# Optimization experiments

Hardware: AMD Instinct MI355X
Metric: run time of the kernel (lower is better)

## Reference

```python
import jax, jax.numpy as jnp
import numpy as np

H = 512; V = 100; V1 = V + 1; T = 20; L = 2; B = 1024; M = 5; K = 10; DFF = 4 * H
NEG = -1e9


def _ln(x, g, b):
    m = x.mean(-1, keepdims=True)
    v = x.var(-1, keepdims=True)
    return (x - m) / jnp.sqrt(v + 1e-5) * g + b


def _attn(q_in, kv_in, iw, ib, ow, ob, mask):
    # single-head attention, inputs [T,B,H] / [S,B,H]
    q = q_in @ iw[:H].T + ib[:H]
    k = kv_in @ iw[H:2 * H].T + ib[H:2 * H]
    v = kv_in @ iw[2 * H:].T + ib[2 * H:]
    s = jnp.einsum('qbh,kbh->bqk', q, k) / jnp.sqrt(jnp.float32(H))
    if mask is not None:
        s = s + mask
    a = jax.nn.softmax(s, axis=-1)
    o = jnp.einsum('bqk,kbh->qbh', a, v)
    return o @ ow.T + ob


def _pos_encoding(max_len, d):
    pos = jnp.arange(max_len, dtype=jnp.float32)[:, None]
    div = jnp.exp(jnp.arange(0, d, 2, dtype=jnp.float32) * (-np.log(10000.0) / d))
    pe = jnp.zeros((max_len, d), jnp.float32)
    pe = pe.at[:, 0::2].set(jnp.sin(pos * div)).at[:, 1::2].set(jnp.cos(pos * div))
    return pe[:, None, :]  # [T,1,H]


def setup_inputs() -> dict:
    key = jax.random.key(0)
    ks = jax.random.split(key, 20)
    s = 0.05
    rn = lambda k, shape: jax.random.normal(k, shape, jnp.float32) * s
    return dict(
        meanings=jax.random.randint(ks[0], (B, M), 0, K),
        emb_table=rn(ks[1], (M * K, H)),
        v2e_w=rn(ks[2], (H, V1)), v2e_b=rn(ks[3], (H,)),
        e2v_w=rn(ks[4], (V1, H)), e2v_b=rn(ks[5], (V1,)),
        sa_in_w=rn(ks[6], (L, 3 * H, H)), sa_in_b=rn(ks[7], (L, 3 * H)),
        sa_out_w=rn(ks[8], (L, H, H)), sa_out_b=rn(ks[9], (L, H)),
        ca_in_w=rn(ks[10], (L, 3 * H, H)), ca_in_b=rn(ks[11], (L, 3 * H)),
        ca_out_w=rn(ks[12], (L, H, H)), ca_out_b=rn(ks[13], (L, H)),
        ff1_w=rn(ks[14], (L, DFF, H)), ff1_b=rn(ks[15], (L, DFF)),
        ff2_w=rn(ks[16], (L, H, DFF)), ff2_b=rn(ks[17], (L, H)),
        ln_g=jnp.ones((L, 3, H), jnp.float32),
        ln_b=jnp.zeros((L, 3, H), jnp.float32),
    )


def reference(meanings, emb_table, v2e_w, v2e_b, e2v_w, e2v_b,
              sa_in_w, sa_in_b, sa_out_w, sa_out_b,
              ca_in_w, ca_in_b, ca_out_w, ca_out_b,
              ff1_w, ff1_b, ff2_w, ff2_b, ln_g, ln_b):
    bsz = meanings.shape[0]
    # meanings_offset = (cumsum(ones)-1)*K == arange(M)*K
    idx = meanings + jnp.arange(M) * K          # [B,M]
    src = emb_table[idx].sum(axis=1)[None]      # [1,B,H] memory
    pe = _pos_encoding(T, H)
    # start token one-hot probabilities
    probs = jnp.zeros((1, bsz, V1), jnp.float32).at[:, :, V].set(1.0)
    outs = []
    for i in range(T):
        x = probs @ v2e_w.T + v2e_b + pe[:i + 1]            # [i+1,B,H]
        mask = jnp.triu(jnp.full((i + 1, i + 1), NEG, jnp.float32), k=1)
        for l in range(L):
            x = _ln(x + _attn(x, x, sa_in_w[l], sa_in_b[l], sa_out_w[l], sa_out_b[l], mask),
                    ln_g[l, 0], ln_b[l, 0])
            x = _ln(x + _attn(x, src, ca_in_w[l], ca_in_b[l], ca_out_w[l], ca_out_b[l], None),
                    ln_g[l, 1], ln_b[l, 1])
            ff = jax.nn.relu(x @ ff1_w[l].T + ff1_b[l]) @ ff2_w[l].T + ff2_b[l]
            x = _ln(x + ff, ln_g[l, 2], ln_b[l, 2])
        logits = x @ e2v_w.T + e2v_b                        # [i+1,B,V1]
        last = logits[-1]                                   # [B,V1]
        outs.append(last)
        probs = jnp.concatenate([probs, jax.nn.softmax(last, axis=-1)[None]], axis=0)
    return jnp.stack(outs, axis=0)                          # [T,B,V1]
```

## Files before the change

### kernel.cpp

```cpp
#include <hip/hip_runtime.h>
#include <hip/hip_bf16.h>
#include <math.h>

#define Hdim 512
#define Vv   100
#define V1n  101
#define Tt   20
#define Ln   2
#define Bb   1024
#define Mm   5
#define Kk   10
#define DFFn 2048

typedef _Float16 f16;
typedef __attribute__((ext_vector_type(8))) _Float16 f16x8;
typedef __attribute__((ext_vector_type(16))) float f32x16;

static const size_t BH  = (size_t)Bb * Hdim;
static const size_t PSP = (size_t)Bb * 128;

__device__ __forceinline__ void split2(float v, f16* s) {
    f16 h0 = (f16)v;
    float r = v - (float)h0;
    s[0] = h0; s[1] = (f16)r;
}
__device__ __forceinline__ void xsp_write(f16* __restrict__ xsp, int row, int h, float v)
{
    f16 s[2]; split2(v, s);
    size_t o = (size_t)(h >> 3) * 8192 + (size_t)row * 8 + (h & 7);
    xsp[o] = s[0]; xsp[BH + o] = s[1];
}

template<int EPI>
__global__ __launch_bounds__(256, 2) void gemm_sp(
    const f16* __restrict__ Asp, const f16* __restrict__ Wsp,
    const float* __restrict__ bias,
    float* __restrict__ C, f16* __restrict__ Csp, size_t cplane,
    int N, int Kd, int kcount, int posn)
{
    __shared__ f16 lds[16384];
    const int tid = threadIdx.x;
    const int lane = tid & 63, w = tid >> 6;
    const int wm = w >> 1, wn = w & 1;
    const int bm = blockIdx.y * 128, bn = blockIdx.x * 128;
    const int kc0 = blockIdx.z * (kcount >> 3);
    const int nt = kcount >> 5;
    const int K8 = Kd >> 3;

    size_t gA[4], gB[4]; int lA[4], lB[4];
#pragma unroll
    for (int q = 0; q < 4; ++q) {
        int cid = q * 256 + tid, slab = cid >> 7, win = cid & 127;
        int p = slab >> 2, kcr = slab & 3;
        gA[q] = ((size_t)p * K8 + kc0 + kcr) * 8192 + (size_t)bm * 8 + win * 8;
        lA[q] = slab * 1024 + win * 8;
        gB[q] = ((size_t)p * K8 + kc0 + kcr) * ((size_t)N * 8) + (size_t)bn * 8 + win * 8;
        lB[q] = 8192 + slab * 1024 + win * 8;
    }

    f32x16 acc[2][2];
#pragma unroll
    for (int mi = 0; mi < 2; ++mi)
#pragma unroll
        for (int ni = 0; ni < 2; ++ni)
#pragma unroll
            for (int j = 0; j < 16; ++j) acc[mi][ni][j] = 0.f;

    f16x8 rA[4], rB[4];
#pragma unroll
    for (int q = 0; q < 4; ++q) {
        rA[q] = *(const f16x8*)(Asp + gA[q]);
        rB[q] = *(const f16x8*)(Wsp + gB[q]);
    }

    for (int t = 0; t < nt; ++t) {
        __syncthreads();
#pragma unroll
        for (int q = 0; q < 4; ++q) {
            *(f16x8*)&lds[lA[q]] = rA[q];
            *(f16x8*)&lds[lB[q]] = rB[q];
        }
        __syncthreads();
        if (t + 1 < nt) {
#pragma unroll
            for (int q = 0; q < 4; ++q) {
                rA[q] = *(const f16x8*)(Asp + gA[q] + (size_t)(t + 1) * 32768);
                rB[q] = *(const f16x8*)(Wsp + gB[q] + (size_t)(t + 1) * 32 * N);
            }
        }
#pragma unroll
        for (int ks = 0; ks < 2; ++ks) {
            const int kb = (2 * ks + (lane >> 5)) * 1024 + (lane & 31) * 8;
            f16x8 a[2][2], b[2][2];
#pragma unroll
            for (int mi = 0; mi < 2; ++mi)
#pragma unroll
                for (int p = 0; p < 2; ++p)
                    a[mi][p] = *(const f16x8*)&lds[p * 4096 + kb + (64 * wm + 32 * mi) * 8];
#pragma unroll
            for (int ni = 0; ni < 2; ++ni)
#pragma unroll
                for (int p = 0; p < 2; ++p)
                    b[ni][p] = *(const f16x8*)&lds[8192 + p * 4096 + kb + (64 * wn + 32 * ni) * 8];
#pragma unroll
            for (int mi = 0; mi < 2; ++mi)
#pragma unroll
                for (int ni = 0; ni < 2; ++ni) {
                    f32x16 v = acc[mi][ni];
                    v = __builtin_amdgcn_mfma_f32_32x32x16_f16(a[mi][1], b[ni][0], v, 0, 0, 0);
                    v = __builtin_amdgcn_mfma_f32_32x32x16_f16(a[mi][0], b[ni][1], v, 0, 0, 0);
                    v = __builtin_amdgcn_mfma_f32_32x32x16_f16(a[mi][0], b[ni][0], v, 0, 0, 0);
                    acc[mi][ni] = v;
                }
        }
    }

    const int er0 = bm + 64 * wm + 4 * (lane >> 5);
    const int ec0 = bn + 64 * wn + (lane & 31);
#pragma unroll
    for (int mi = 0; mi < 2; ++mi) {
#pragma unroll
        for (int ni = 0; ni < 2; ++ni) {
            int col = ec0 + 32 * ni;
#pragma unroll
            for (int r = 0; r < 16; ++r) {
                int row = er0 + 32 * mi + (r & 3) + 8 * (r >> 2);
                float v = acc[mi][ni][r];
                if (EPI == 0) {
                    C[(size_t)blockIdx.z * Bb * N + (size_t)row * N + col] = v;
                } else if (EPI == 1) {
                    v = fmaxf(v + bias[col], 0.f);
                    f16 s[2]; split2(v, s);
                    size_t o = (size_t)(col >> 3) * 8192 + (size_t)row * 8 + (col & 7);
                    Csp[o] = s[0]; Csp[cplane + o] = s[1];
                } else if (EPI == 3) {
                    v += bias[col];
                    f16 s[2]; split2(v, s);
                    size_t o = (size_t)(col >> 3) * 8192 + (size_t)row * 8 + (col & 7);
                    Csp[o] = s[0]; Csp[cplane + o] = s[1];
                } else if (EPI == 4) {
                    C[(size_t)row * N + col] = v + bias[col];
                } else if (EPI == 5) {
                    v += bias[col];
                    int j2 = col & ~1;
                    float div = expf(-(float)j2 * (logf(10000.f) / (float)Hdim));
                    float ang = (float)posn * div;
                    v += (col & 1) ? cosf(ang) : sinf(ang);
                    C[(size_t)row * Hdim + col] = v;
                    f16 s[2]; split2(v, s);
                    size_t o = (size_t)(col >> 3) * 8192 + (size_t)row * 8 + (col & 7);
                    Csp[o] = s[0]; Csp[cplane + o] = s[1];
                }
            }
        }
    }
}

__global__ void split_mat(const float* __restrict__ src, f16* __restrict__ dst,
                          int Nreal, int Npad, int Kreal, int kpl)
{
    int i = blockIdx.x * 256 + threadIdx.x;
    int Kpad = 1 << kpl;
    if (i >= (Npad << kpl)) return;
    int n = i >> kpl, k = i & (Kpad - 1);
    float v = (n < Nreal && k < Kreal) ? src[(size_t)n * Kreal + k] : 0.f;
    f16 s[2]; split2(v, s);
    size_t plane = (size_t)Npad << kpl;
    size_t o = (size_t)(k >> 3) * ((size_t)Npad * 8) + (size_t)n * 8 + (k & 7);
    dst[o] = s[0]; dst[plane + o] = s[1];
}

__global__ void src_kernel(const int* __restrict__ meanings,
                           const float* __restrict__ emb, f16* __restrict__ ssp)
{
    int idx = blockIdx.x * 256 + threadIdx.x;
    int b = idx >> 9, h = idx & 511;
    float s = 0.f;
#pragma unroll
    for (int m = 0; m < Mm; ++m) {
        int row = meanings[b * Mm + m] + m * Kk;
        s += emb[(size_t)row * Hdim + h];
    }
    xsp_write(ssp, b, h, s);
}

__global__ void init_x(const float* __restrict__ v2e_w, const float* __restrict__ v2e_b,
                       float* __restrict__ x, f16* __restrict__ xsp)
{
    int idx = blockIdx.x * 256 + threadIdx.x;
    int b = idx >> 9, h = idx & 511;
    float s = v2e_w[(size_t)h * V1n + Vv] + v2e_b[h] + ((h & 1) ? 1.f : 0.f);
    x[idx] = s;
    xsp_write(xsp, b, h, s);
}

__global__ __launch_bounds__(256) void attn_fused(
    const float* __restrict__ P, const float* __restrict__ bias3h,
    float* __restrict__ kc, float* __restrict__ vc,
    f16* __restrict__ osplit, int step)
{
    __shared__ float qs[Hdim];
    __shared__ float ssm[32];
    __shared__ float wts[32];
    int b = blockIdx.x, tid = threadIdx.x, lane = tid & 63, wv = tid >> 6;
    const size_t PS = (size_t)Bb * 1536;
    const float* pb = P + (size_t)b * 1536;
#pragma unroll
    for (int c0 = 0; c0 < 2; ++c0) {
        int c = tid + c0 * 256;
        float qv = bias3h[c]        + pb[c]        + pb[PS + c];
        float kv = bias3h[512 + c]  + pb[512 + c]  + pb[PS + 512 + c];
        float vv = bias3h[1024 + c] + pb[1024 + c] + pb[PS + 1024 + c];
        qs[c] = qv;
        kc[((size_t)step * Bb + b) * Hdim + c] = kv;
        vc[((size_t)step * Bb + b) * Hdim + c] = vv;
    }
    __syncthreads();
    const float4* q4 = (const float4*)qs;
    for (int t = wv; t <= step; t += 4) {
        const float4* k4 = (const float4*)(kc + ((size_t)t * Bb + b) * Hdim);
        float4 qa = q4[lane], ka = k4[lane];
        float4 qb = q4[lane + 64], kb = k4[lane + 64];
        float p = qa.x*ka.x + qa.y*ka.y + qa.z*ka.z + qa.w*ka.w
                + qb.x*kb.x + qb.y*kb.y + qb.z*kb.z + qb.w*kb.w;
#pragma unroll
        for (int off = 32; off; off >>= 1) p += __shfl_down(p, off);
        if (!lane) ssm[t] = p * 0.044194173824159216f;
    }
    __syncthreads();
    float m = -1e30f;
    for (int t = 0; t <= step; ++t) m = fmaxf(m, ssm[t]);
    float den = 0.f;
    for (int t = 0; t <= step; ++t) den += expf(ssm[t] - m);
    if (tid <= step) wts[tid] = expf(ssm[tid] - m) / den;
    __syncthreads();
#pragma unroll
    for (int c0 = 0; c0 < 2; ++c0) {
        int h = tid + c0 * 256;
        float a2 = 0.f;
        for (int t = 0; t <= step; ++t)
            a2 += wts[t] * vc[((size_t)t * Bb + b) * Hdim + h];
        xsp_write(osplit, b, h, a2);
    }
}

__device__ __forceinline__ float2 rowstats(float v0, float v1, float* sh)
{
    __syncthreads();
    float s = v0 + v1, s2 = v0 * v0 + v1 * v1;
    int lane = threadIdx.x & 63, wv = threadIdx.x >> 6;
#pragma unroll
    for (int off = 32; off; off >>= 1) {
        s += __shfl_down(s, off);
        s2 += __shfl_down(s2, off);
    }
    if (!lane) { sh[wv] = s; sh[wv + 4] = s2; }
    __syncthreads();
    float S = sh[0] + sh[1] + sh[2] + sh[3];
    float S2 = sh[4] + sh[5] + sh[6] + sh[7];
    float mean = S * (1.f / Hdim);
    float var = S2 * (1.f / Hdim) - mean * mean;
    return make_float2(mean, rsqrtf(var + 1e-5f));
}

template<int NZ>
__global__ __launch_bounds__(256) void ln12(
    float* __restrict__ x, const float* __restrict__ P, const float* __restrict__ ob,
    const float* __restrict__ cross,
    const float* __restrict__ g0, const float* __restrict__ b0,
    const float* __restrict__ g1, const float* __restrict__ b1,
    f16* __restrict__ xsp)
{
    __shared__ float sh[8];
    size_t base = (size_t)blockIdx.x * Hdim;
    int tid = threadIdx.x;
    float v0 = x[base + tid] + ob[tid];
    float v1 = x[base + tid + 256] + ob[tid + 256];
#pragma unroll
    for (int z = 0; z < NZ; ++z) {
        v0 += P[z * BH + base + tid];
        v1 += P[z * BH + base + tid + 256];
    }
    float2 st = rowstats(v0, v1, sh);
    float y0 = (v0 - st.x) * st.y * g0[tid] + b0[tid] + cross[base + tid];
    float y1 = (v1 - st.x) * st.y * g0[tid + 256] + b0[tid + 256] + cross[base + tid + 256];
    float2 s2 = rowstats(y0, y1, sh);
    float o0 = (y0 - s2.x) * s2.y * g1[tid] + b1[tid];
    float o1 = (y1 - s2.x) * s2.y * g1[tid + 256] + b1[tid + 256];
    x[base + tid] = o0; x[base + tid + 256] = o1;
    xsp_write(xsp, blockIdx.x, tid, o0);
    xsp_write(xsp, blockIdx.x, tid + 256, o1);
}

template<int NZ>
__global__ __launch_bounds__(256) void ln3(
    float* __restrict__ x, const float* __restrict__ P, const float* __restrict__ fb,
    const float* __restrict__ g, const float* __restrict__ bbv, f16* __restrict__ xsp)
{
    __shared__ float sh[8];
    size_t base = (size_t)blockIdx.x * Hdim;
    int tid = threadIdx.x;
    float v0 = x[base + tid] + fb[tid];
    float v1 = x[base + tid + 256] + fb[tid + 256];
#pragma unroll
    for (int z = 0; z < NZ; ++z) {
        v0 += P[z * BH + base + tid];
        v1 += P[z * BH + base + tid + 256];
    }
    float2 st = rowstats(v0, v1, sh);
    float o0 = (v0 - st.x) * st.y * g[tid] + bbv[tid];
    float o1 = (v1 - st.x) * st.y * g[tid + 256] + bbv[tid + 256];
    x[base + tid] = o0; x[base + tid + 256] = o1;
    xsp_write(xsp, blockIdx.x, tid, o0);
    xsp_write(xsp, blockIdx.x, tid + 256, o1);
}

__global__ __launch_bounds__(128) void softmax_out(
    const float* __restrict__ P, const float* __restrict__ e2v_b,
    float* __restrict__ out_i, f16* __restrict__ psp)
{
    __shared__ float red[4];
    int b = blockIdx.x, v = threadIdx.x, lane = v & 63, wv = v >> 6;
    bool valid = v < V1n;
    float s = -1e30f;
    if (valid) {
        s = e2v_b[v];
#pragma unroll
        for (int z = 0; z < 4; ++z) s += P[(size_t)z * Bb * 128 + (size_t)b * 128 + v];
        out_i[(size_t)b * V1n + v] = s;
    }
    float m = s;
#pragma unroll
    for (int off = 32; off; off >>= 1) m = fmaxf(m, __shfl_xor(m, off));
    if (!lane) red[wv] = m;
    __syncthreads();
    float M = fmaxf(red[0], red[1]);
    float e = valid ? expf(s - M) : 0.f;
    float d = e;
#pragma unroll
    for (int off = 32; off; off >>= 1) d += __shfl_xor(d, off);
    if (!lane) red[2 + wv] = d;
    __syncthreads();
    float D = red[2] + red[3];
    float p = valid ? e / D : 0.f;
    f16 t2[2]; split2(p, t2);
    size_t o = (size_t)(v >> 3) * 8192 + (size_t)b * 8 + (v & 7);
    psp[o] = t2[0]; psp[PSP + o] = t2[1];
}

extern "C" void kernel_launch(void* const* d_in, const int* in_sizes, int n_in,
                              void* d_out, int out_size, void* d_ws, size_t ws_size,
                              hipStream_t stream)
{
    const int*   meanings = (const int*)  d_in[0];
    const float* emb      = (const float*)d_in[1];
    const float* v2e_w    = (const float*)d_in[2];
    const float* v2e_b    = (const float*)d_in[3];
    const float* e2v_w    = (const float*)d_in[4];
    const float* e2v_b    = (const float*)d_in[5];
    const float* sa_in_w  = (const float*)d_in[6];
    const float* sa_in_b  = (const float*)d_in[7];
    const float* sa_out_w = (const float*)d_in[8];
    const float* sa_out_b = (const float*)d_in[9];
    const float* ca_in_w  = (const float*)d_in[10];
    const float* ca_in_b  = (const float*)d_in[11];
    const float* ca_out_w = (const float*)d_in[12];
    const float* ca_out_b = (const float*)d_in[13];
    const float* ff1_w    = (const float*)d_in[14];
    const float* ff1_b    = (const float*)d_in[15];
    const float* ff2_w    = (const float*)d_in[16];
    const float* ff2_b    = (const float*)d_in[17];
    const float* ln_g     = (const float*)d_in[18];
    const float* ln_b     = (const float*)d_in[19];
    float* out = (float*)d_out;

    char* wsb = (char*)d_ws;
    auto alloc = [&](size_t bytes) {
        char* p = wsb; wsb += (bytes + 255) & ~(size_t)255; return p;
    };
    const int nsain = 1536 * 512, nsaout = 512 * 512, nff1 = 2048 * 512,
              nff2 = 512 * 2048, nca = 512 * 512;
    f16 *wsp_sa_in[2], *wsp_sa_out[2], *wsp_ff1[2], *wsp_ff2[2];
    for (int l = 0; l < 2; ++l) wsp_sa_in[l]  = (f16*)alloc((size_t)2 * nsain * 2);
    for (int l = 0; l < 2; ++l) wsp_sa_out[l] = (f16*)alloc((size_t)2 * nsaout * 2);
    for (int l = 0; l < 2; ++l) wsp_ff1[l]    = (f16*)alloc((size_t)2 * nff1 * 2);
    for (int l = 0; l < 2; ++l) wsp_ff2[l]    = (f16*)alloc((size_t)2 * nff2 * 2);
    float* x       = (float*)alloc(BH * 4);
    f16*   xsp     = (f16*)  alloc(2 * BH * 2);
    float* cross   = (float*)alloc(2 * BH * 4);
    float* Pbuf    = (float*)alloc(8 * BH * 4);
    f16*   h1sp    = (f16*)  alloc(2 * (size_t)Bb * DFFn * 2);
    f16*   psp     = (f16*)  alloc(2 * PSP * 2);
    f16*   e2v_wsp = (f16*)  alloc((size_t)2 * 128 * 512 * 2);
    f16*   v2e_wsp = (f16*)  alloc((size_t)2 * 512 * 128 * 2);
    float* kc      = (float*)alloc((size_t)Ln * Tt * BH * 4);
    float* vc      = (float*)alloc((size_t)Ln * Tt * BH * 4);
    f16* ssp    = h1sp;
    f16* wspc_v = (f16*)Pbuf;
    f16* wspc_o = wspc_v + (size_t)2 * nca;
    f16* vssp   = wspc_o + (size_t)2 * nca;

    const float* srcs[8] = { sa_in_w, sa_in_w + nsain, sa_out_w, sa_out_w + nsaout,
                             ff1_w, ff1_w + nff1, ff2_w, ff2_w + nff2 };
    f16* dsts[8] = { wsp_sa_in[0], wsp_sa_in[1], wsp_sa_out[0], wsp_sa_out[1],
                     wsp_ff1[0], wsp_ff1[1], wsp_ff2[0], wsp_ff2[1] };
    int nN[8] = { 1536, 1536, 512, 512, 2048, 2048, 512, 512 };
    int kb[8] = { 9, 9, 9, 9, 9, 9, 11, 11 };
    for (int i = 0; i < 8; ++i)
        split_mat<<<(nN[i] << kb[i]) / 256, 256, 0, stream>>>(
            srcs[i], dsts[i], nN[i], nN[i], 1 << kb[i], kb[i]);
    split_mat<<<(128 << 9) / 256, 256, 0, stream>>>(e2v_w, e2v_wsp, V1n, 128, 512, 9);
    split_mat<<<(512 << 7) / 256, 256, 0, stream>>>(v2e_w, v2e_wsp, 512, 512, V1n, 7);

    src_kernel<<<BH / 256, 256, 0, stream>>>(meanings, emb, ssp);
    for (int l = 0; l < Ln; ++l) {
        split_mat<<<nca / 256, 256, 0, stream>>>(
            ca_in_w + (size_t)l * 3 * Hdim * Hdim + (size_t)2 * Hdim * Hdim,
            wspc_v, 512, 512, 512, 9);
        split_mat<<<nca / 256, 256, 0, stream>>>(
            ca_out_w + (size_t)l * Hdim * Hdim, wspc_o, 512, 512, 512, 9);
        gemm_sp<3><<<dim3(4, 8, 1), 256, 0, stream>>>(
            ssp, wspc_v, ca_in_b + l * 1536 + 1024,
            nullptr, vssp, BH, 512, 512, 512, 0);
        gemm_sp<4><<<dim3(4, 8, 1), 256, 0, stream>>>(
            vssp, wspc_o, ca_out_b + l * 512,
            cross + (size_t)l * BH, nullptr, 0, 512, 512, 512, 0);
    }
    init_x<<<BH / 256, 256, 0, stream>>>(v2e_w, v2e_b, x, xsp);

    for (int i = 0; i < Tt; ++i) {
        for (int l = 0; l < Ln; ++l) {
            float* kcl = kc + (size_t)l * Tt * BH;
            float* vcl = vc + (size_t)l * Tt * BH;
            gemm_sp<0><<<dim3(12, 8, 2), 256, 0, stream>>>(
                xsp, wsp_sa_in[l], nullptr,
                Pbuf, nullptr, 0, 1536, 512, 256, 0);
            attn_fused<<<Bb, 256, 0, stream>>>(Pbuf, sa_in_b + l * 1536,
                                               kcl, vcl, xsp, i);
            gemm_sp<0><<<dim3(4, 8, 8), 256, 0, stream>>>(
                xsp, wsp_sa_out[l], nullptr,
                Pbuf, nullptr, 0, 512, 512, 64, 0);
            ln12<8><<<Bb, 256, 0, stream>>>(x, Pbuf, sa_out_b + l * 512,
                cross + (size_t)l * BH,
                ln_g + (size_t)(l * 3 + 0) * Hdim, ln_b + (size_t)(l * 3 + 0) * Hdim,
                ln_g + (size_t)(l * 3 + 1) * Hdim, ln_b + (size_t)(l * 3 + 1) * Hdim,
                xsp);
            gemm_sp<1><<<dim3(16, 8, 1), 256, 0, stream>>>(
                xsp, wsp_ff1[l], ff1_b + l * 2048,
                nullptr, h1sp, (size_t)Bb * DFFn, 2048, 512, 512, 0);
            gemm_sp<0><<<dim3(4, 8, 8), 256, 0, stream>>>(
                h1sp, wsp_ff2[l], nullptr,
                Pbuf, nullptr, 0, 512, 2048, 256, 0);
            ln3<8><<<Bb, 256, 0, stream>>>(x, Pbuf, ff2_b + l * 512,
                ln_g + (size_t)(l * 3 + 2) * Hdim, ln_b + (size_t)(l * 3 + 2) * Hdim,
                xsp);
        }
        gemm_sp<0><<<dim3(1, 8, 4), 256, 0, stream>>>(
            xsp, e2v_wsp, nullptr, Pbuf, nullptr, 0, 128, 512, 128, 0);
        softmax_out<<<Bb, 128, 0, stream>>>(
            Pbuf, e2v_b, out + (size_t)i * Bb * V1n, psp);
        if (i + 1 < Tt)
            gemm_sp<5><<<dim3(4, 8, 1), 256, 0, stream>>>(
                psp, v2e_wsp, v2e_b, x, xsp, BH, 512, 128, 128, i + 1);
    }
}
```

Baseline: 3.727 ms.

## Load GEMM A-fragments from global, fuse logits/softmax/embed into one kernel

The split-fp16 GEMM now reads A operand fragments straight from global memory into registers and stages only B in LDS, halving shared memory and dropping the launch_bounds occupancy hint. The per-step tail (e2v logits GEMM, softmax, v2e embedding GEMM with positional encoding) is replaced by a single fp32 CUDA-core kernel over 8 rows per block, with transposed fp32 weights. This removes three launches per step and the split-precision conversions for the small GEMMs, but the fused kernel runs only 128 blocks, and the A loads lose coalescing and LDS reuse across waves.

```diff
diff --git a/kernel.cpp b/kernel.cpp
--- a/kernel.cpp
+++ b/kernel.cpp
@@ -16,8 +16,7 @@
 typedef __attribute__((ext_vector_type(8))) _Float16 f16x8;
 typedef __attribute__((ext_vector_type(16))) float f32x16;
 
-static const size_t BH  = (size_t)Bb * Hdim;
-static const size_t PSP = (size_t)Bb * 128;
+static const size_t BH = (size_t)Bb * Hdim;
 
 __device__ __forceinline__ void split2(float v, f16* s) {
     f16 h0 = (f16)v;
@@ -32,13 +31,13 @@
 }
 
 template<int EPI>
-__global__ __launch_bounds__(256, 2) void gemm_sp(
+__global__ __launch_bounds__(256) void gemm_sp(
     const f16* __restrict__ Asp, const f16* __restrict__ Wsp,
     const float* __restrict__ bias,
     float* __restrict__ C, f16* __restrict__ Csp, size_t cplane,
-    int N, int Kd, int kcount, int posn)
-{
-    __shared__ f16 lds[16384];
+    int N, int Kd, int kcount)
+{
+    __shared__ f16 ldsB[8192];
     const int tid = threadIdx.x;
     const int lane = tid & 63, w = tid >> 6;
     const int wm = w >> 1, wn = w & 1;
@@ -46,17 +45,19 @@
     const int kc0 = blockIdx.z * (kcount >> 3);
     const int nt = kcount >> 5;
     const int K8 = Kd >> 3;
-
-    size_t gA[4], gB[4]; int lA[4], lB[4];
+    const int rl = lane & 31, kl = lane >> 5;
+
+    size_t gB[4]; int lB[4];
 #pragma unroll
     for (int q = 0; q < 4; ++q) {
         int cid = q * 256 + tid, slab = cid >> 7, win = cid & 127;
         int p = slab >> 2, kcr = slab & 3;
-        gA[q] = ((size_t)p * K8 + kc0 + kcr) * 8192 + (size_t)bm * 8 + win * 8;
-        lA[q] = slab * 1024 + win * 8;
-        gB[q] = ((size_t)p * K8 + kc0 + kcr) * ((size_t)N * 8) + (size_t)bn * 8 + win * 8;
-        lB[q] = 8192 + slab * 1024 + win * 8;
-    }
+        gB[q] = ((size_t)(p * K8 + kc0 + kcr)) * ((size_t)N * 8) + (size_t)(bn + win) * 8;
+        lB[q] = slab * 1024 + win * 8;
+    }
+    const size_t abase = (size_t)(bm + 64 * wm + rl) * 8;
+    const size_t kb0 = (size_t)(kc0 + kl) * 8192;
+    const size_t kpl = (size_t)K8 * 8192;
 
     f32x16 acc[2][2];
 #pragma unroll
@@ -66,50 +67,46 @@
 #pragma unroll
             for (int j = 0; j < 16; ++j) acc[mi][ni][j] = 0.f;
 
-    f16x8 rA[4], rB[4];
-#pragma unroll
-    for (int q = 0; q < 4; ++q) {
-        rA[q] = *(const f16x8*)(Asp + gA[q]);
-        rB[q] = *(const f16x8*)(Wsp + gB[q]);
-    }
+    f16x8 rB[4];
+#pragma unroll
+    for (int q = 0; q < 4; ++q) rB[q] = *(const f16x8*)(Wsp + gB[q]);
 
     for (int t = 0; t < nt; ++t) {
         __syncthreads();
 #pragma unroll
-        for (int q = 0; q < 4; ++q) {
-            *(f16x8*)&lds[lA[q]] = rA[q];
-            *(f16x8*)&lds[lB[q]] = rB[q];
+        for (int q = 0; q < 4; ++q) *(f16x8*)&ldsB[lB[q]] = rB[q];
+        __syncthreads();
+        f16x8 aF[2][2][2];
+#pragma unroll
+        for (int ks = 0; ks < 2; ++ks)
+#pragma unroll
+            for (int mi = 0; mi < 2; ++mi)
+#pragma unroll
+                for (int p = 0; p < 2; ++p)
+                    aF[ks][mi][p] = *(const f16x8*)(Asp + (size_t)p * kpl + kb0
+                                     + (size_t)(4 * t + 2 * ks) * 8192 + abase + mi * 256);
+        if (t + 1 < nt) {
+#pragma unroll
+            for (int q = 0; q < 4; ++q)
+                rB[q] = *(const f16x8*)(Wsp + gB[q] + (size_t)(t + 1) * 32 * N);
         }
-        __syncthreads();
-        if (t + 1 < nt) {
-#pragma unroll
-            for (int q = 0; q < 4; ++q) {
-                rA[q] = *(const f16x8*)(Asp + gA[q] + (size_t)(t + 1) * 32768);
-                rB[q] = *(const f16x8*)(Wsp + gB[q] + (size_t)(t + 1) * 32 * N);
-            }
-        }
 #pragma unroll
         for (int ks = 0; ks < 2; ++ks) {
-            const int kb = (2 * ks + (lane >> 5)) * 1024 + (lane & 31) * 8;
-            f16x8 a[2][2], b[2][2];
-#pragma unroll
-            for (int mi = 0; mi < 2; ++mi)
+            f16x8 b[2][2];
+#pragma unroll
+            for (int ni = 0; ni < 2; ++ni)
 #pragma unroll
                 for (int p = 0; p < 2; ++p)
-                    a[mi][p] = *(const f16x8*)&lds[p * 4096 + kb + (64 * wm + 32 * mi) * 8];
-#pragma unroll
-            for (int ni = 0; ni < 2; ++ni)
-#pragma unroll
-                for (int p = 0; p < 2; ++p)
-                    b[ni][p] = *(const f16x8*)&lds[8192 + p * 4096 + kb + (64 * wn + 32 * ni) * 8];
+                    b[ni][p] = *(const f16x8*)&ldsB[p * 4096 + (2 * ks + kl) * 1024
+                                 + (64 * wn + 32 * ni + rl) * 8];
 #pragma unroll
             for (int mi = 0; mi < 2; ++mi)
 #pragma unroll
                 for (int ni = 0; ni < 2; ++ni) {
                     f32x16 v = acc[mi][ni];
-                    v = __builtin_amdgcn_mfma_f32_32x32x16_f16(a[mi][1], b[ni][0], v, 0, 0, 0);
-                    v = __builtin_amdgcn_mfma_f32_32x32x16_f16(a[mi][0], b[ni][1], v, 0, 0, 0);
-                    v = __builtin_amdgcn_mfma_f32_32x32x16_f16(a[mi][0], b[ni][0], v, 0, 0, 0);
+                    v = __builtin_amdgcn_mfma_f32_32x32x16_f16(aF[ks][mi][1], b[ni][0], v, 0, 0, 0);
+                    v = __builtin_amdgcn_mfma_f32_32x32x16_f16(aF[ks][mi][0], b[ni][1], v, 0, 0, 0);
+                    v = __builtin_amdgcn_mfma_f32_32x32x16_f16(aF[ks][mi][0], b[ni][0], v, 0, 0, 0);
                     acc[mi][ni] = v;
                 }
         }
@@ -138,18 +135,8 @@
                     f16 s[2]; split2(v, s);
                     size_t o = (size_t)(col >> 3) * 8192 + (size_t)row * 8 + (col & 7);
                     Csp[o] = s[0]; Csp[cplane + o] = s[1];
-                } else if (EPI == 4) {
+                } else {
                     C[(size_t)row * N + col] = v + bias[col];
-                } else if (EPI == 5) {
-                    v += bias[col];
-                    int j2 = col & ~1;
-                    float div = expf(-(float)j2 * (logf(10000.f) / (float)Hdim));
-                    float ang = (float)posn * div;
-                    v += (col & 1) ? cosf(ang) : sinf(ang);
-                    C[(size_t)row * Hdim + col] = v;
-                    f16 s[2]; split2(v, s);
-                    size_t o = (size_t)(col >> 3) * 8192 + (size_t)row * 8 + (col & 7);
-                    Csp[o] = s[0]; Csp[cplane + o] = s[1];
                 }
             }
         }
@@ -157,17 +144,29 @@
 }
 
 __global__ void split_mat(const float* __restrict__ src, f16* __restrict__ dst,
-                          int Nreal, int Npad, int Kreal, int kpl)
+                          int Nn, int kbits)
 {
     int i = blockIdx.x * 256 + threadIdx.x;
-    int Kpad = 1 << kpl;
-    if (i >= (Npad << kpl)) return;
-    int n = i >> kpl, k = i & (Kpad - 1);
-    float v = (n < Nreal && k < Kreal) ? src[(size_t)n * Kreal + k] : 0.f;
-    f16 s[2]; split2(v, s);
-    size_t plane = (size_t)Npad << kpl;
-    size_t o = (size_t)(k >> 3) * ((size_t)Npad * 8) + (size_t)n * 8 + (k & 7);
+    int Kd = 1 << kbits;
+    if (i >= (Nn << kbits)) return;
+    int n = i >> kbits, k = i & (Kd - 1);
+    f16 s[2]; split2(src[i], s);
+    size_t plane = (size_t)Nn << kbits;
+    size_t o = (size_t)(k >> 3) * ((size_t)Nn * 8) + (size_t)n * 8 + (k & 7);
     dst[o] = s[0]; dst[plane + o] = s[1];
+}
+
+__global__ void transpose_e2v(const float* __restrict__ w, float* __restrict__ wT)
+{
+    int i = blockIdx.x * 256 + threadIdx.x;
+    int h = i >> 7, v = i & 127;
+    wT[i] = (v < V1n) ? w[(size_t)v * Hdim + h] : 0.f;
+}
+__global__ void transpose_v2e(const float* __restrict__ w, float* __restrict__ wT)
+{
+    int i = blockIdx.x * 256 + threadIdx.x;
+    int v = i >> 9, h = i & 511;
+    wT[i] = (v < V1n) ? w[(size_t)h * V1n + v] : 0.f;
 }
 
 __global__ void src_kernel(const int* __restrict__ meanings,
@@ -263,7 +262,6 @@
     return make_float2(mean, rsqrtf(var + 1e-5f));
 }
 
-template<int NZ>
 __global__ __launch_bounds__(256) void ln12(
     float* __restrict__ x, const float* __restrict__ P, const float* __restrict__ ob,
     const float* __restrict__ cross,
@@ -277,7 +275,7 @@
     float v0 = x[base + tid] + ob[tid];
     float v1 = x[base + tid + 256] + ob[tid + 256];
 #pragma unroll
-    for (int z = 0; z < NZ; ++z) {
+    for (int z = 0; z < 8; ++z) {
         v0 += P[z * BH + base + tid];
         v1 += P[z * BH + base + tid + 256];
     }
@@ -292,7 +290,6 @@
     xsp_write(xsp, blockIdx.x, tid + 256, o1);
 }
 
-template<int NZ>
 __global__ __launch_bounds__(256) void ln3(
     float* __restrict__ x, const float* __restrict__ P, const float* __restrict__ fb,
     const float* __restrict__ g, const float* __restrict__ bbv, f16* __restrict__ xsp)
@@ -303,7 +300,7 @@
     float v0 = x[base + tid] + fb[tid];
     float v1 = x[base + tid + 256] + fb[tid + 256];
 #pragma unroll
-    for (int z = 0; z < NZ; ++z) {
+    for (int z = 0; z < 8; ++z) {
         v0 += P[z * BH + base + tid];
         v1 += P[z * BH + base + tid + 256];
     }
@@ -315,37 +312,103 @@
     xsp_write(xsp, blockIdx.x, tid + 256, o1);
 }
 
-__global__ __launch_bounds__(128) void softmax_out(
-    const float* __restrict__ P, const float* __restrict__ e2v_b,
-    float* __restrict__ out_i, f16* __restrict__ psp)
-{
-    __shared__ float red[4];
-    int b = blockIdx.x, v = threadIdx.x, lane = v & 63, wv = v >> 6;
-    bool valid = v < V1n;
-    float s = -1e30f;
-    if (valid) {
-        s = e2v_b[v];
-#pragma unroll
-        for (int z = 0; z < 4; ++z) s += P[(size_t)z * Bb * 128 + (size_t)b * 128 + v];
-        out_i[(size_t)b * V1n + v] = s;
-    }
-    float m = s;
-#pragma unroll
-    for (int off = 32; off; off >>= 1) m = fmaxf(m, __shfl_xor(m, off));
-    if (!lane) red[wv] = m;
-    __syncthreads();
-    float M = fmaxf(red[0], red[1]);
-    float e = valid ? expf(s - M) : 0.f;
-    float d = e;
-#pragma unroll
-    for (int off = 32; off; off >>= 1) d += __shfl_xor(d, off);
-    if (!lane) red[2 + wv] = d;
-    __syncthreads();
-    float D = red[2] + red[3];
-    float p = valid ? e / D : 0.f;
-    f16 t2[2]; split2(p, t2);
-    size_t o = (size_t)(v >> 3) * 8192 + (size_t)b * 8 + (v & 7);
-    psp[o] = t2[0]; psp[PSP + o] = t2[1];
+__global__ __launch_bounds__(256) void finish_fused(
+    const float* __restrict__ xin, const float* __restrict__ e2v_wT,
+    const float* __restrict__ e2v_b, const float* __restrict__ v2e_wT,
+    const float* __restrict__ v2e_b, float* __restrict__ out_i,
+    float* __restrict__ x, f16* __restrict__ xsp, int pos_next, int upd)
+{
+    __shared__ float xs[8][512];
+    __shared__ float ls[8][104];
+    int tid = threadIdx.x;
+    int b0 = blockIdx.x * 8;
+#pragma unroll
+    for (int r = 0; r < 8; ++r) {
+        xs[r][tid] = xin[(size_t)(b0 + r) * Hdim + tid];
+        xs[r][tid + 256] = xin[(size_t)(b0 + r) * Hdim + tid + 256];
+    }
+    if (tid < 24) { int r = tid / 3; ls[r][101 + tid % 3] = 0.f; }
+    __syncthreads();
+
+    int row = tid >> 5, vl = tid & 31;
+    float lg0 = 0.f, lg1 = 0.f, lg2 = 0.f, lg3 = 0.f;
+#pragma unroll 8
+    for (int h = 0; h < 512; ++h) {
+        float xv = xs[row][h];
+        const float* wr = e2v_wT + h * 128 + vl;
+        lg0 += xv * wr[0];  lg1 += xv * wr[32];
+        lg2 += xv * wr[64]; lg3 += xv * wr[96];
+    }
+    float lg[4] = { lg0, lg1, lg2, lg3 };
+#pragma unroll
+    for (int rep = 0; rep < 4; ++rep) {
+        int v = vl + 32 * rep;
+        if (v < V1n) {
+            float val = lg[rep] + e2v_b[v];
+            ls[row][v] = val;
+            out_i[(size_t)(b0 + row) * V1n + v] = val;
+        }
+    }
+    __syncthreads();
+    if (!upd) return;
+
+    {
+        float a0 = ls[row][vl];
+        float a1 = (vl + 32 < V1n) ? ls[row][vl + 32] : -1e30f;
+        float a2 = (vl + 64 < V1n) ? ls[row][vl + 64] : -1e30f;
+        float a3 = (vl + 96 < V1n) ? ls[row][vl + 96] : -1e30f;
+        float m = fmaxf(fmaxf(a0, a1), fmaxf(a2, a3));
+#pragma unroll
+        for (int off = 16; off; off >>= 1) m = fmaxf(m, __shfl_xor(m, off));
+        float e0 = expf(a0 - m);
+        float e1 = (vl + 32 < V1n) ? expf(a1 - m) : 0.f;
+        float e2 = (vl + 64 < V1n) ? expf(a2 - m) : 0.f;
+        float e3 = (vl + 96 < V1n) ? expf(a3 - m) : 0.f;
+        float s = e0 + e1 + e2 + e3;
+#pragma unroll
+        for (int off = 16; off; off >>= 1) s += __shfl_xor(s, off);
+        float inv = 1.f / s;
+        ls[row][vl] = e0 * inv;
+        if (vl + 32 < V1n) ls[row][vl + 32] = e1 * inv;
+        if (vl + 64 < V1n) ls[row][vl + 64] = e2 * inv;
+        if (vl + 96 < V1n) ls[row][vl + 96] = e3 * inv;
+    }
+    __syncthreads();
+
+    float acc0[8], acc1[8];
+#pragma unroll
+    for (int r = 0; r < 8; ++r) { acc0[r] = 0.f; acc1[r] = 0.f; }
+    for (int vc = 0; vc < 104; vc += 8) {
+        float w0[8], w1[8];
+#pragma unroll
+        for (int j = 0; j < 8; ++j) {
+            w0[j] = v2e_wT[(size_t)(vc + j) * 512 + tid];
+            w1[j] = v2e_wT[(size_t)(vc + j) * 512 + tid + 256];
+        }
+#pragma unroll
+        for (int r = 0; r < 8; ++r)
+#pragma unroll
+            for (int j = 0; j < 8; ++j) {
+                float p = ls[r][vc + j];
+                acc0[r] += p * w0[j];
+                acc1[r] += p * w1[j];
+            }
+    }
+    int h0 = tid, h1 = tid + 256;
+    const float cpe = logf(10000.f) / (float)Hdim;
+    float d0 = expf(-(float)(h0 & ~1) * cpe), d1 = expf(-(float)(h1 & ~1) * cpe);
+    float pe0 = (h0 & 1) ? cosf((float)pos_next * d0) : sinf((float)pos_next * d0);
+    float pe1 = (h1 & 1) ? cosf((float)pos_next * d1) : sinf((float)pos_next * d1);
+    float vb0 = v2e_b[h0], vb1 = v2e_b[h1];
+#pragma unroll
+    for (int r = 0; r < 8; ++r) {
+        float s0 = acc0[r] + vb0 + pe0;
+        float s1 = acc1[r] + vb1 + pe1;
+        x[(size_t)(b0 + r) * Hdim + h0] = s0;
+        x[(size_t)(b0 + r) * Hdim + h1] = s1;
+        xsp_write(xsp, b0 + r, h0, s0);
+        xsp_write(xsp, b0 + r, h1, s1);
+    }
 }
 
 extern "C" void kernel_launch(void* const* d_in, const int* in_sizes, int n_in,
@@ -390,9 +453,8 @@
     float* cross   = (float*)alloc(2 * BH * 4);
     float* Pbuf    = (float*)alloc(8 * BH * 4);
     f16*   h1sp    = (f16*)  alloc(2 * (size_t)Bb * DFFn * 2);
-    f16*   psp     = (f16*)  alloc(2 * PSP * 2);
-    f16*   e2v_wsp = (f16*)  alloc((size_t)2 * 128 * 512 * 2);
-    f16*   v2e_wsp = (f16*)  alloc((size_t)2 * 512 * 128 * 2);
+    float* e2v_wT  = (float*)alloc((size_t)512 * 128 * 4);
+    float* v2e_wT  = (float*)alloc((size_t)128 * 512 * 4);
     float* kc      = (float*)alloc((size_t)Ln * Tt * BH * 4);
     float* vc      = (float*)alloc((size_t)Ln * Tt * BH * 4);
     f16* ssp    = h1sp;
@@ -407,24 +469,22 @@
     int nN[8] = { 1536, 1536, 512, 512, 2048, 2048, 512, 512 };
     int kb[8] = { 9, 9, 9, 9, 9, 9, 11, 11 };
     for (int i = 0; i < 8; ++i)
-        split_mat<<<(nN[i] << kb[i]) / 256, 256, 0, stream>>>(
-            srcs[i], dsts[i], nN[i], nN[i], 1 << kb[i], kb[i]);
-    split_mat<<<(128 << 9) / 256, 256, 0, stream>>>(e2v_w, e2v_wsp, V1n, 128, 512, 9);
-    split_mat<<<(512 << 7) / 256, 256, 0, stream>>>(v2e_w, v2e_wsp, 512, 512, V1n, 7);
+        split_mat<<<(nN[i] << kb[i]) / 256, 256, 0, stream>>>(srcs[i], dsts[i], nN[i], kb[i]);
+    transpose_e2v<<<(512 * 128) / 256, 256, 0, stream>>>(e2v_w, e2v_wT);
+    transpose_v2e<<<(128 * 512) / 256, 256, 0, stream>>>(v2e_w, v2e_wT);
 
     src_kernel<<<BH / 256, 256, 0, stream>>>(meanings, emb, ssp);
     for (int l = 0; l < Ln; ++l) {
         split_mat<<<nca / 256, 256, 0, stream>>>(
-            ca_in_w + (size_t)l * 3 * Hdim * Hdim + (size_t)2 * Hdim * Hdim,
-            wspc_v, 512, 512, 512, 9);
+            ca_in_w + (size_t)l * 3 * Hdim * Hdim + (size_t)2 * Hdim * Hdim, wspc_v, 512, 9);
         split_mat<<<nca / 256, 256, 0, stream>>>(
-            ca_out_w + (size_t)l * Hdim * Hdim, wspc_o, 512, 512, 512, 9);
+            ca_out_w + (size_t)l * Hdim * Hdim, wspc_o, 512, 9);
         gemm_sp<3><<<dim3(4, 8, 1), 256, 0, stream>>>(
             ssp, wspc_v, ca_in_b + l * 1536 + 1024,
-            nullptr, vssp, BH, 512, 512, 512, 0);
+            nullptr, vssp, BH, 512, 512, 512);
         gemm_sp<4><<<dim3(4, 8, 1), 256, 0, stream>>>(
             vssp, wspc_o, ca_out_b + l * 512,
-            cross + (size_t)l * BH, nullptr, 0, 512, 512, 512, 0);
+            cross + (size_t)l * BH, nullptr, 0, 512, 512, 512);
     }
     init_x<<<BH / 256, 256, 0, stream>>>(v2e_w, v2e_b, x, xsp);
 
@@ -434,33 +494,29 @@
             float* vcl = vc + (size_t)l * Tt * BH;
             gemm_sp<0><<<dim3(12, 8, 2), 256, 0, stream>>>(
                 xsp, wsp_sa_in[l], nullptr,
-                Pbuf, nullptr, 0, 1536, 512, 256, 0);
+                Pbuf, nullptr, 0, 1536, 512, 256);
             attn_fused<<<Bb, 256, 0, stream>>>(Pbuf, sa_in_b + l * 1536,
                                                kcl, vcl, xsp, i);
             gemm_sp<0><<<dim3(4, 8, 8), 256, 0, stream>>>(
                 xsp, wsp_sa_out[l], nullptr,
-                Pbuf, nullptr, 0, 512, 512, 64, 0);
-            ln12<8><<<Bb, 256, 0, stream>>>(x, Pbuf, sa_out_b + l * 512,
+                Pbuf, nullptr, 0, 512, 512, 64);
+            ln12<<<Bb, 256, 0, stream>>>(x, Pbuf, sa_out_b + l * 512,
                 cross + (size_t)l * BH,
                 ln_g + (size_t)(l * 3 + 0) * Hdim, ln_b + (size_t)(l * 3 + 0) * Hdim,
                 ln_g + (size_t)(l * 3 + 1) * Hdim, ln_b + (size_t)(l * 3 + 1) * Hdim,
                 xsp);
             gemm_sp<1><<<dim3(16, 8, 1), 256, 0, stream>>>(
                 xsp, wsp_ff1[l], ff1_b + l * 2048,
-                nullptr, h1sp, (size_t)Bb * DFFn, 2048, 512, 512, 0);
+                nullptr, h1sp, (size_t)Bb * DFFn, 2048, 512, 512);
             gemm_sp<0><<<dim3(4, 8, 8), 256, 0, stream>>>(
                 h1sp, wsp_ff2[l], nullptr,
-                Pbuf, nullptr, 0, 512, 2048, 256, 0);
-            ln3<8><<<Bb, 256, 0, stream>>>(x, Pbuf, ff2_b + l * 512,
+                Pbuf, nullptr, 0, 512, 2048, 256);
+            ln3<<<Bb, 256, 0, stream>>>(x, Pbuf, ff2_b + l * 512,
                 ln_g + (size_t)(l * 3 + 2) * Hdim, ln_b + (size_t)(l * 3 + 2) * Hdim,
                 xsp);
         }
-        gemm_sp<0><<<dim3(1, 8, 4), 256, 0, stream>>>(
-            xsp, e2v_wsp, nullptr, Pbuf, nullptr, 0, 128, 512, 128, 0);
-        softmax_out<<<Bb, 128, 0, stream>>>(
-            Pbuf, e2v_b, out + (size_t)i * Bb * V1n, psp);
-        if (i + 1 < Tt)
-            gemm_sp<5><<<dim3(4, 8, 1), 256, 0, stream>>>(
-                psp, v2e_wsp, v2e_b, x, xsp, BH, 512, 128, 128, i + 1);
-    }
-}
+        finish_fused<<<128, 256, 0, stream>>>(
+            x, e2v_wT, e2v_b, v2e_wT, v2e_b,
+            out + (size_t)i * Bb * V1n, x, xsp, i + 1, (i + 1 < Tt) ? 1 : 0);
+    }
+}
```

After: 5.006 ms. 1.34x slower.
